# Kernel optimization log

Hardware: AMD Instinct MI355X
Metric: run time of the kernel (lower is better)

Reference implementation:

```python
import jax, jax.numpy as jnp
import numpy as np

DIM = 192
NUM_HEADS = 6
HEAD_DIM = DIM // NUM_HEADS
WS = 8            # window_size
SHIFT = 4         # shift_size
SCALE = HEAD_DIM ** -0.5


def window_partition(x, ws):
    # x: (B, H, W, C) -> (B*nWh*nWw, ws, ws, C)
    B, H, W, C = x.shape
    x = x.reshape(B, H // ws, ws, W // ws, ws, C)
    x = x.transpose(0, 1, 3, 2, 4, 5)
    return x.reshape(-1, ws, ws, C)


def window_reverse(windows, ws, H, W):
    C = windows.shape[-1]
    B = windows.shape[0] // ((H // ws) * (W // ws))
    x = windows.reshape(B, H // ws, W // ws, ws, ws, C)
    x = x.transpose(0, 1, 3, 2, 4, 5)
    return x.reshape(B, H, W, C)


def depthwise_conv3x3(x, w, b):
    # x: (N, H, W, C), w: (3, 3, 1, C) HWIO with feature_group_count=C
    y = jax.lax.conv_general_dilated(
        x, w, window_strides=(1, 1), padding='SAME',
        dimension_numbers=('NHWC', 'HWIO', 'NHWC'),
        feature_group_count=x.shape[-1])
    return y + b


def setup_inputs() -> dict:
    key = jax.random.key(0)
    ks = jax.random.split(key, 5)
    B, H, W = 4, 128, 128
    WB = B * (H // WS) * (W // WS)  # 1024 windows
    N = WS * WS                      # 64 tokens per window
    x = jax.random.normal(ks[0], (B, H, W, DIM), dtype=jnp.float32)
    prev_attn_map = jax.random.uniform(ks[1], (WB, NUM_HEADS, N, N), dtype=jnp.float32)
    qkv_w = jax.random.normal(ks[2], (DIM, 3 * DIM), dtype=jnp.float32) * 0.02
    qkv_b = jnp.zeros((3 * DIM,), dtype=jnp.float32)
    proj_w = jax.random.normal(ks[3], (DIM, DIM), dtype=jnp.float32) * 0.02
    proj_b = jnp.zeros((DIM,), dtype=jnp.float32)
    lepe_w = jax.random.normal(ks[4], (3, 3, 1, DIM), dtype=jnp.float32) * 0.02
    lepe_b = jnp.zeros((DIM,), dtype=jnp.float32)
    return {'x': x, 'prev_attn_map': prev_attn_map, 'qkv_w': qkv_w, 'qkv_b': qkv_b,
            'proj_w': proj_w, 'proj_b': proj_b, 'lepe_w': lepe_w, 'lepe_b': lepe_b}


def reference(x, prev_attn_map, qkv_w, qkv_b, proj_w, proj_b, lepe_w, lepe_b):
    B, H, W, C = x.shape
    N = WS * WS
    # shifted window partition
    shifted = jnp.roll(x, shift=(-SHIFT, -SHIFT), axis=(1, 2))
    xw = window_partition(shifted, WS)              # (WB, ws, ws, C)
    WB = xw.shape[0]
    xw = xw.reshape(WB, N, C)
    # QKV projection
    qkv = xw @ qkv_w + qkv_b                        # (WB, N, 3C)
    qkv = qkv.reshape(WB, N, 3, NUM_HEADS, HEAD_DIM).transpose(2, 0, 3, 1, 4)
    q, k, v = qkv[0], qkv[1], qkv[2]                # (WB, nh, N, hd)
    # LePE: depthwise conv on v in 2D window layout
    v_2d = v.transpose(0, 2, 1, 3).reshape(WB, WS, WS, C)
    lepe_v = depthwise_conv3x3(v_2d, lepe_w, lepe_b)
    lepe_v = lepe_v.reshape(WB, N, NUM_HEADS, HEAD_DIM).transpose(0, 2, 1, 3)
    v = v + lepe_v
    # attention with inherited-map Hadamard gating
    attn_scores = jnp.einsum('bhqd,bhkd->bhqk', q, k) * SCALE
    attn_scores = attn_scores * prev_attn_map       # progressive focusing
    attn = jax.nn.softmax(attn_scores, axis=-1)     # (WB, nh, N, N)
    out = jnp.einsum('bhqk,bhkd->bhqd', attn, v)
    out = out.transpose(0, 2, 1, 3).reshape(WB, N, C)
    out = out @ proj_w + proj_b
    # reverse windows and unshift
    out = window_reverse(out.reshape(WB, WS, WS, C), WS, H, W)
    out = jnp.roll(out, shift=(SHIFT, SHIFT), axis=(1, 2))
    return out, attn
```

## Files before the change

### kernel.cpp

```cpp
#include <hip/hip_runtime.h>


#define SCALE 0.17677669529663687f

typedef __attribute__((ext_vector_type(8))) short short8;
typedef __attribute__((ext_vector_type(4))) float f32x4;

__device__ __forceinline__ unsigned short f2bf(float f) {
    unsigned int u = __float_as_uint(f);
    u = (u + 0x7FFFu + ((u >> 16) & 1u)) >> 16;
    return (unsigned short)u;
}
__device__ __forceinline__ float bf2f(unsigned short h) {
    return __uint_as_float(((unsigned int)h) << 16);
}
__device__ __forceinline__ unsigned int pack2(float a, float b) {
    return (unsigned int)f2bf(a) | ((unsigned int)f2bf(b) << 16);
}

__global__ __launch_bounds__(256) void k0_pack(const float* __restrict__ qkv_w,
                                               const float* __restrict__ proj_w,
                                               unsigned short* __restrict__ qkvp,
                                               unsigned short* __restrict__ projp) {
    int gid = blockIdx.x * 256 + threadIdx.x;
    if (gid < 6 * 36 * 64) {
        int lane = gid & 63, tile = gid >> 6;
        int nt = tile % 36, ks = tile / 36;
        int row = ks * 32 + (lane >> 4) * 8, col = nt * 16 + (lane & 15);
        const float* w = qkv_w + (size_t)row * 576 + col;
        uint4 o;
        o.x = pack2(w[0 * 576], w[1 * 576]);
        o.y = pack2(w[2 * 576], w[3 * 576]);
        o.z = pack2(w[4 * 576], w[5 * 576]);
        o.w = pack2(w[6 * 576], w[7 * 576]);
        *(uint4*)(qkvp + (size_t)gid * 8) = o;
    } else {
        int g = gid - 6 * 36 * 64;
        int lane = g & 63, tile = g >> 6;
        int nt = tile % 12, ks = tile / 12;
        int row = ks * 32 + (lane >> 4) * 8, col = nt * 16 + (lane & 15);
        const float* w = proj_w + (size_t)row * 192 + col;
        uint4 o;
        o.x = pack2(w[0 * 192], w[1 * 192]);
        o.y = pack2(w[2 * 192], w[3 * 192]);
        o.z = pack2(w[4 * 192], w[5 * 192]);
        o.w = pack2(w[6 * 192], w[7 * 192]);
        *(uint4*)(projp + (size_t)g * 8) = o;
    }
}

#define LDS_QK 0
#define LDS_VT 24576

__global__ __launch_bounds__(384, 3) void k_fused(
    const float* __restrict__ x, const float* __restrict__ prev,
    const float* __restrict__ qkv_b, const float* __restrict__ lepe_w,
    const float* __restrict__ lepe_b, const float* __restrict__ proj_b,
    const unsigned short* __restrict__ qkvp, const unsigned short* __restrict__ projp,
    float* __restrict__ out, float* __restrict__ attn)
{
    __shared__ unsigned short lds[38400];
    const int wb = blockIdx.x;
    const int b = wb >> 8, wh = (wb >> 4) & 15, wwi = wb & 15;
    const int t = threadIdx.x;
    const int lane = t & 63, h = t >> 6, quad = lane >> 4, l16 = lane & 15;
    const f32x4 fz = {0.f, 0.f, 0.f, 0.f};

#pragma unroll
    for (int kk = 0; kk < 8; ++kk) {
        int f = kk * 384 + t;
        int token = f / 48, c4 = f - token * 48;
        int i = token >> 3, j = token & 7;
        int hh = (wh * 8 + i + 4) & 127, wp = (wwi * 8 + j + 4) & 127;
        const float4 v4 = *(const float4*)(x + ((size_t)((b * 128 + hh) * 128 + wp)) * 192 + c4 * 4);
        unsigned int* d = (unsigned int*)&lds[token * 200 + c4 * 4];
        d[0] = pack2(v4.x, v4.y);
        d[1] = pack2(v4.z, v4.w);
    }
    __syncthreads();

    const int ntg[6] = {2 * h, 2 * h + 1, 12 + 2 * h, 13 + 2 * h, 24 + 2 * h, 25 + 2 * h};

    unsigned short* qh  = &lds[LDS_QK + h * 4096];
    unsigned short* kh  = qh + 2048;
    unsigned short* vth = &lds[LDS_VT + h * 2304];

    {
        f32x4 acc[6][4];
#pragma unroll
        for (int j = 0; j < 6; ++j)
#pragma unroll
            for (int m = 0; m < 4; ++m) acc[j][m] = fz;

#pragma unroll
        for (int ks = 0; ks < 6; ++ks) {
            short8 a[4];
#pragma unroll
            for (int m = 0; m < 4; ++m)
                a[m] = *(const short8*)&lds[(m * 16 + l16) * 200 + ks * 32 + quad * 8];
#pragma unroll
            for (int j = 0; j < 6; ++j) {
                short8 bf = *(const short8*)(qkvp + (((size_t)(ks * 36 + ntg[j]) * 64 + lane) << 3));
#pragma unroll
                for (int m = 0; m < 4; ++m)
                    acc[j][m] = __builtin_amdgcn_mfma_f32_16x16x32_bf16(a[m], bf, acc[j][m], 0, 0, 0);
            }
        }
        __syncthreads();

#pragma unroll
        for (int j = 0; j < 6; ++j) {
            float bias = qkv_b[ntg[j] * 16 + l16];
#pragma unroll
            for (int m = 0; m < 4; ++m) {
#pragma unroll
                for (int r = 0; r < 4; ++r) {
                    int token = m * 16 + quad * 4 + r;
                    unsigned short bv = f2bf(acc[j][m][r] + bias);
                    if (j < 2)      qh[token * 32 + j * 16 + l16] = bv;
                    else if (j < 4) kh[token * 32 + (j - 2) * 16 + l16] = bv;
                    else            vth[((j - 4) * 16 + l16) * 72 + token] = bv;
                }
            }
        }
    }
    __syncthreads();

    {
        const int ti = lane >> 3, tj = lane & 7;
        for (int ci = 0; ci < 32; ++ci) {
            int c = h * 32 + ci;
            const unsigned short* vr = vth + ci * 72;
            float sum = bf2f(vr[lane]) + lepe_b[c];
#pragma unroll
            for (int di = -1; di <= 1; ++di)
#pragma unroll
                for (int dj = -1; dj <= 1; ++dj) {
                    int ii = ti + di, jj = tj + dj;
                    if (ii >= 0 && ii < 8 && jj >= 0 && jj < 8)
                        sum += bf2f(vr[ii * 8 + jj]) * lepe_w[((di + 1) * 3 + (dj + 1)) * 192 + c];
                }
            vth[ci * 72 + lane] = f2bf(sum);
        }
    }

    f32x4 s4[4][4];
    {
        short8 aq[4];
#pragma unroll
        for (int m = 0; m < 4; ++m)
            aq[m] = *(const short8*)(qh + (m * 16 + l16) * 32 + quad * 8);
#pragma unroll
        for (int nt = 0; nt < 4; ++nt) {
            short8 bk = *(const short8*)(kh + (nt * 16 + l16) * 32 + quad * 8);
#pragma unroll
            for (int m = 0; m < 4; ++m)
                s4[m][nt] = __builtin_amdgcn_mfma_f32_16x16x32_bf16(aq[m], bk, fz, 0, 0, 0);
        }
    }

    const float* pvm = prev + (((size_t)wb * 6 + h) << 12);
    float* aom = attn + (((size_t)wb * 6 + h) << 12);
    unsigned short* Ph = qh;
#pragma unroll
    for (int m = 0; m < 4; ++m) {
        float e[4][4], inv[4];
#pragma unroll
        for (int r = 0; r < 4; ++r) {
            int row = m * 16 + quad * 4 + r;
            float ps = 0.f;
#pragma unroll
            for (int nt = 0; nt < 4; ++nt) {
                float sg = s4[m][nt][r] * SCALE * pvm[row * 64 + nt * 16 + l16];
                float ev = __expf(sg);
                e[r][nt] = ev; ps += ev;
            }
            ps += __shfl_xor(ps, 1); ps += __shfl_xor(ps, 2);
            ps += __shfl_xor(ps, 4); ps += __shfl_xor(ps, 8);
            inv[r] = 1.0f / ps;
        }
#pragma unroll
        for (int r = 0; r < 4; ++r) {
            int row = m * 16 + quad * 4 + r;
#pragma unroll
            for (int nt = 0; nt < 4; ++nt) {
                float av = e[r][nt] * inv[r];
                aom[row * 64 + nt * 16 + l16] = av;
                Ph[row * 64 + nt * 16 + l16] = f2bf(av);
            }
        }
    }
    __syncthreads();

    {
        f32x4 o2[4][2];
#pragma unroll
        for (int m = 0; m < 4; ++m) { o2[m][0] = fz; o2[m][1] = fz; }
#pragma unroll
        for (int ks = 0; ks < 2; ++ks) {
            short8 ap[4];
#pragma unroll
            for (int m = 0; m < 4; ++m)
                ap[m] = *(const short8*)(Ph + (m * 16 + l16) * 64 + ks * 32 + quad * 8);
#pragma unroll
            for (int n2 = 0; n2 < 2; ++n2) {
                short8 bv = *(const short8*)(vth + (n2 * 16 + l16) * 72 + ks * 32 + quad * 8);
#pragma unroll
                for (int m = 0; m < 4; ++m)
                    o2[m][n2] = __builtin_amdgcn_mfma_f32_16x16x32_bf16(ap[m], bv, o2[m][n2], 0, 0, 0);
            }
        }
        unsigned short* oh = vth;
#pragma unroll
        for (int m = 0; m < 4; ++m)
#pragma unroll
            for (int n2 = 0; n2 < 2; ++n2)
#pragma unroll
                for (int r = 0; r < 4; ++r)
                    oh[(m * 16 + quad * 4 + r) * 32 + n2 * 16 + l16] = f2bf(o2[m][n2][r]);
    }
    __syncthreads();

    {
        f32x4 p3[2][4];
#pragma unroll
        for (int n = 0; n < 2; ++n)
#pragma unroll
            for (int m = 0; m < 4; ++m) p3[n][m] = fz;

#pragma unroll
        for (int ks = 0; ks < 6; ++ks) {
            const unsigned short* ob = &lds[LDS_VT + ks * 2304];
            short8 a3[4];
#pragma unroll
            for (int m = 0; m < 4; ++m)
                a3[m] = *(const short8*)(ob + (m * 16 + l16) * 32 + quad * 8);
#pragma unroll
            for (int n = 0; n < 2; ++n) {
                short8 bf = *(const short8*)(projp + (((size_t)(ks * 12 + h * 2 + n) * 64 + lane) << 3));
#pragma unroll
                for (int m = 0; m < 4; ++m)
                    p3[n][m] = __builtin_amdgcn_mfma_f32_16x16x32_bf16(a3[m], bf, p3[n][m], 0, 0, 0);
            }
        }
#pragma unroll
        for (int n = 0; n < 2; ++n) {
            int col = (h * 2 + n) * 16 + l16;
            float bias = proj_b[col];
#pragma unroll
            for (int m = 0; m < 4; ++m)
#pragma unroll
                for (int r = 0; r < 4; ++r) {
                    int token = m * 16 + quad * 4 + r;
                    int i = token >> 3, j = token & 7;
                    int hh = (wh * 8 + i + 4) & 127, wp = (wwi * 8 + j + 4) & 127;
                    out[((size_t)((b * 128 + hh) * 128 + wp)) * 192 + col] = p3[n][m][r] + bias;
                }
        }
    }
}

extern "C" void kernel_launch(void* const* d_in, const int* in_sizes, int n_in,
                              void* d_out, int out_size, void* d_ws, size_t ws_size,
                              hipStream_t stream) {
    const float* x      = (const float*)d_in[0];
    const float* prev   = (const float*)d_in[1];
    const float* qkv_w  = (const float*)d_in[2];
    const float* qkv_b  = (const float*)d_in[3];
    const float* proj_w = (const float*)d_in[4];
    const float* proj_b = (const float*)d_in[5];
    const float* lepe_w = (const float*)d_in[6];
    const float* lepe_b = (const float*)d_in[7];

    float* out  = (float*)d_out;
    float* attn = out + (size_t)4 * 128 * 128 * 192;

    char* ws = (char*)d_ws;
    const size_t SZ_QKVP = 192 * 576 * 2;
    unsigned short* qkvp  = (unsigned short*)(ws);
    unsigned short* projp = (unsigned short*)(ws + SZ_QKVP);

    k0_pack<<<72, 256, 0, stream>>>(qkv_w, proj_w, qkvp, projp);
    k_fused<<<1024, 384, 0, stream>>>(x, prev, qkv_b, lepe_w, lepe_b, proj_b,
                                      qkvp, projp, out, attn);
}
```

Baseline: 398.8 us.

## Compact per-head LDS regions and drop intermediate barriers to shrink shared memory

Shared memory is reorganised into per-head regions in which V-transpose reuses the Q slot, and P and O share a small buffer, cutting the allocation from about 77KB to about 52KB. Several block-wide __syncthreads are removed because each wave now touches only its own region. QK^T is computed before the V scatter, and P is written to LDS in two halves for the PV MMA. The aim is higher occupancy and fewer barriers, at the cost of tighter buffer aliasing and some added LDS writes.

```diff
diff --git a/kernel.cpp b/kernel.cpp
--- a/kernel.cpp
+++ b/kernel.cpp
@@ -49,8 +49,9 @@
     }
 }
 
-#define LDS_QK 0
-#define LDS_VT 24576
+#define RH 4352
+#define KO 2048
+#define PO 2304
 
 __global__ __launch_bounds__(384, 3) void k_fused(
     const float* __restrict__ x, const float* __restrict__ prev,
@@ -59,7 +60,7 @@
     const unsigned short* __restrict__ qkvp, const unsigned short* __restrict__ projp,
     float* __restrict__ out, float* __restrict__ attn)
 {
-    __shared__ unsigned short lds[38400];
+    __shared__ unsigned short lds[26112];
     const int wb = blockIdx.x;
     const int b = wb >> 8, wh = (wb >> 4) & 15, wwi = wb & 15;
     const int t = threadIdx.x;
@@ -80,51 +81,75 @@
     __syncthreads();
 
     const int ntg[6] = {2 * h, 2 * h + 1, 12 + 2 * h, 13 + 2 * h, 24 + 2 * h, 25 + 2 * h};
-
-    unsigned short* qh  = &lds[LDS_QK + h * 4096];
-    unsigned short* kh  = qh + 2048;
-    unsigned short* vth = &lds[LDS_VT + h * 2304];
-
+    unsigned short* qh  = &lds[h * RH];
+    unsigned short* kh  = qh + KO;
+    unsigned short* vth = qh;
+    unsigned short* Pf  = qh + PO;
+
+    f32x4 acc[6][4];
+#pragma unroll
+    for (int j = 0; j < 6; ++j)
+#pragma unroll
+        for (int m = 0; m < 4; ++m) acc[j][m] = fz;
+
+#pragma unroll
+    for (int ks = 0; ks < 6; ++ks) {
+        short8 a[4];
+#pragma unroll
+        for (int m = 0; m < 4; ++m)
+            a[m] = *(const short8*)&lds[(m * 16 + l16) * 200 + ks * 32 + quad * 8];
+#pragma unroll
+        for (int j = 0; j < 6; ++j) {
+            short8 bf = *(const short8*)(qkvp + (((size_t)(ks * 36 + ntg[j]) * 64 + lane) << 3));
+#pragma unroll
+            for (int m = 0; m < 4; ++m)
+                acc[j][m] = __builtin_amdgcn_mfma_f32_16x16x32_bf16(a[m], bf, acc[j][m], 0, 0, 0);
+        }
+    }
+    __syncthreads();
+
+#pragma unroll
+    for (int j = 0; j < 4; ++j) {
+        float bias = qkv_b[ntg[j] * 16 + l16];
+        unsigned short* base = (j < 2) ? qh : kh;
+#pragma unroll
+        for (int m = 0; m < 4; ++m) {
+#pragma unroll
+            for (int r = 0; r < 4; ++r) {
+                int token = m * 16 + quad * 4 + r;
+                base[token * 32 + (j & 1) * 16 + l16] = f2bf(acc[j][m][r] + bias);
+            }
+        }
+    }
+
+    f32x4 s4[4][4];
     {
-        f32x4 acc[6][4];
-#pragma unroll
-        for (int j = 0; j < 6; ++j)
-#pragma unroll
-            for (int m = 0; m < 4; ++m) acc[j][m] = fz;
-
-#pragma unroll
-        for (int ks = 0; ks < 6; ++ks) {
-            short8 a[4];
-#pragma unroll
-            for (int m = 0; m < 4; ++m)
-                a[m] = *(const short8*)&lds[(m * 16 + l16) * 200 + ks * 32 + quad * 8];
-#pragma unroll
-            for (int j = 0; j < 6; ++j) {
-                short8 bf = *(const short8*)(qkvp + (((size_t)(ks * 36 + ntg[j]) * 64 + lane) << 3));
-#pragma unroll
-                for (int m = 0; m < 4; ++m)
-                    acc[j][m] = __builtin_amdgcn_mfma_f32_16x16x32_bf16(a[m], bf, acc[j][m], 0, 0, 0);
-            }
-        }
-        __syncthreads();
-
-#pragma unroll
-        for (int j = 0; j < 6; ++j) {
-            float bias = qkv_b[ntg[j] * 16 + l16];
-#pragma unroll
-            for (int m = 0; m < 4; ++m) {
-#pragma unroll
-                for (int r = 0; r < 4; ++r) {
-                    int token = m * 16 + quad * 4 + r;
-                    unsigned short bv = f2bf(acc[j][m][r] + bias);
-                    if (j < 2)      qh[token * 32 + j * 16 + l16] = bv;
-                    else if (j < 4) kh[token * 32 + (j - 2) * 16 + l16] = bv;
-                    else            vth[((j - 4) * 16 + l16) * 72 + token] = bv;
-                }
-            }
-        }
-    }
-    __syncthreads();
+        short8 aq[4];
+#pragma unroll
+        for (int m = 0; m < 4; ++m)
+            aq[m] = *(const short8*)(qh + (m * 16 + l16) * 32 + quad * 8);
+#pragma unroll
+        for (int nt = 0; nt < 4; ++nt) {
+            short8 bk = *(const short8*)(kh + (nt * 16 + l16) * 32 + quad * 8);
+#pragma unroll
+            for (int m = 0; m < 4; ++m)
+                s4[m][nt] = __builtin_amdgcn_mfma_f32_16x16x32_bf16(aq[m], bk, fz, 0, 0, 0);
+        }
+    }
+
+#pragma unroll
+    for (int j = 4; j < 6; ++j) {
+        float bias = qkv_b[ntg[j] * 16 + l16];
+        int ch = (j - 4) * 16 + l16;
+#pragma unroll
+        for (int m = 0; m < 4; ++m) {
+#pragma unroll
+            for (int r = 0; r < 4; ++r) {
+                int token = m * 16 + quad * 4 + r;
+                vth[ch * 72 + token] = f2bf(acc[j][m][r] + bias);
+            }
+        }
+    }
 
     {
         const int ti = lane >> 3, tj = lane & 7;
@@ -144,27 +169,11 @@
         }
     }
 
-    f32x4 s4[4][4];
-    {
-        short8 aq[4];
-#pragma unroll
-        for (int m = 0; m < 4; ++m)
-            aq[m] = *(const short8*)(qh + (m * 16 + l16) * 32 + quad * 8);
-#pragma unroll
-        for (int nt = 0; nt < 4; ++nt) {
-            short8 bk = *(const short8*)(kh + (nt * 16 + l16) * 32 + quad * 8);
-#pragma unroll
-            for (int m = 0; m < 4; ++m)
-                s4[m][nt] = __builtin_amdgcn_mfma_f32_16x16x32_bf16(aq[m], bk, fz, 0, 0, 0);
-        }
-    }
-
     const float* pvm = prev + (((size_t)wb * 6 + h) << 12);
     float* aom = attn + (((size_t)wb * 6 + h) << 12);
-    unsigned short* Ph = qh;
 #pragma unroll
     for (int m = 0; m < 4; ++m) {
-        float e[4][4], inv[4];
+        float inv[4];
 #pragma unroll
         for (int r = 0; r < 4; ++r) {
             int row = m * 16 + quad * 4 + r;
@@ -173,7 +182,7 @@
             for (int nt = 0; nt < 4; ++nt) {
                 float sg = s4[m][nt][r] * SCALE * pvm[row * 64 + nt * 16 + l16];
                 float ev = __expf(sg);
-                e[r][nt] = ev; ps += ev;
+                s4[m][nt][r] = ev; ps += ev;
             }
             ps += __shfl_xor(ps, 1); ps += __shfl_xor(ps, 2);
             ps += __shfl_xor(ps, 4); ps += __shfl_xor(ps, 8);
@@ -184,40 +193,49 @@
             int row = m * 16 + quad * 4 + r;
 #pragma unroll
             for (int nt = 0; nt < 4; ++nt) {
-                float av = e[r][nt] * inv[r];
+                float av = s4[m][nt][r] * inv[r];
+                s4[m][nt][r] = av;
                 aom[row * 64 + nt * 16 + l16] = av;
-                Ph[row * 64 + nt * 16 + l16] = f2bf(av);
-            }
-        }
-    }
-    __syncthreads();
+            }
+        }
+    }
 
     {
         f32x4 o2[4][2];
 #pragma unroll
         for (int m = 0; m < 4; ++m) { o2[m][0] = fz; o2[m][1] = fz; }
 #pragma unroll
-        for (int ks = 0; ks < 2; ++ks) {
+        for (int half = 0; half < 2; ++half) {
+#pragma unroll
+            for (int m = 0; m < 4; ++m)
+#pragma unroll
+                for (int nt2 = 0; nt2 < 2; ++nt2)
+#pragma unroll
+                    for (int r = 0; r < 4; ++r) {
+                        int row = m * 16 + quad * 4 + r;
+                        Pf[row * 32 + nt2 * 16 + l16] = f2bf(s4[m][half * 2 + nt2][r]);
+                    }
             short8 ap[4];
 #pragma unroll
             for (int m = 0; m < 4; ++m)
-                ap[m] = *(const short8*)(Ph + (m * 16 + l16) * 64 + ks * 32 + quad * 8);
+                ap[m] = *(const short8*)(Pf + (m * 16 + l16) * 32 + quad * 8);
 #pragma unroll
             for (int n2 = 0; n2 < 2; ++n2) {
-                short8 bv = *(const short8*)(vth + (n2 * 16 + l16) * 72 + ks * 32 + quad * 8);
+                short8 bv = *(const short8*)(vth + (n2 * 16 + l16) * 72 + half * 32 + quad * 8);
 #pragma unroll
                 for (int m = 0; m < 4; ++m)
                     o2[m][n2] = __builtin_amdgcn_mfma_f32_16x16x32_bf16(ap[m], bv, o2[m][n2], 0, 0, 0);
             }
         }
-        unsigned short* oh = vth;
 #pragma unroll
         for (int m = 0; m < 4; ++m)
 #pragma unroll
             for (int n2 = 0; n2 < 2; ++n2)
 #pragma unroll
-                for (int r = 0; r < 4; ++r)
-                    oh[(m * 16 + quad * 4 + r) * 32 + n2 * 16 + l16] = f2bf(o2[m][n2][r]);
+                for (int r = 0; r < 4; ++r) {
+                    int token = m * 16 + quad * 4 + r;
+                    Pf[token * 32 + n2 * 16 + l16] = f2bf(o2[m][n2][r]);
+                }
     }
     __syncthreads();
 
@@ -230,7 +248,7 @@
 
 #pragma unroll
         for (int ks = 0; ks < 6; ++ks) {
-            const unsigned short* ob = &lds[LDS_VT + ks * 2304];
+            const unsigned short* ob = &lds[ks * RH + PO];
             short8 a3[4];
 #pragma unroll
             for (int m = 0; m < 4; ++m)
```

After: 396.0 us. About the same (-0.7%).
